# Optimization experiments

Hardware: AMD Instinct MI355X
Metric: run time of the kernel (lower is better)

Reference implementation:

```python
import jax, jax.numpy as jnp
import numpy as np

B, W, D, R = 8, 1024, 1024, 64
GAMMA_MIN, GAMMA_MAX, ALPHA_CAP, EPS = 0.15, 1.0, 1.0, 1e-8


def _linear_init(key, fan_in, shape):
    bound = 1.0 / np.sqrt(fan_in)
    return jax.random.uniform(key, shape, jnp.float32, -bound, bound)


def setup_inputs() -> dict:
    key = jax.random.key(0)
    ks = jax.random.split(key, 12)
    h = jax.random.normal(ks[0], (B, W, D), jnp.float32)
    # k_base init as in __init__: exp(-0.15*max(j-i,0)) * tril, row-normalized
    pos = jnp.arange(W, dtype=jnp.float32)
    dist_ji = jnp.clip(pos[None, :] - pos[:, None], 0.0)
    causal = jnp.tril(jnp.ones((W, W), jnp.float32))
    k_init = jnp.exp(-0.15 * dist_ji) * causal
    k_base = k_init / jnp.clip(k_init.sum(axis=1, keepdims=True), 1e-8)
    # decay_logit init: gammas in [0.95, 0.995] -> inverse sigmoid of normalized gamma
    gammas = jnp.linspace(0.95, 0.995, R)
    graw = jnp.clip((gammas - GAMMA_MIN) / (GAMMA_MAX - GAMMA_MIN), 1e-6, 1 - 1e-6)
    decay_logit = jnp.log(graw / (1.0 - graw))
    return {
        "h": h,
        "k_base": k_base,
        "decay_logit": decay_logit,
        "gate_logit": jnp.asarray(8.0, jnp.float32),
        "alpha_logit": jnp.asarray(0.0, jnp.float32),
        "u": 0.05 * jax.random.normal(ks[1], (D, R), jnp.float32),
        "v": 0.05 * jax.random.normal(ks[2], (D, R), jnp.float32),
        "proj_w": _linear_init(ks[3], D, (D, D)),
        "proj_b": _linear_init(ks[4], D, (D,)),
        "norm1_scale": jnp.ones((D,), jnp.float32),
        "norm2_scale": jnp.ones((D,), jnp.float32),
        "up_w": _linear_init(ks[5], D, (2 * D, D)),
        "up_b": _linear_init(ks[6], D, (2 * D,)),
        "down_w": _linear_init(ks[7], 2 * D, (D, 2 * D)),
        "down_b": _linear_init(ks[8], 2 * D, (D,)),
    }


def _rmsnorm(x, scale):
    return x * jax.lax.rsqrt(jnp.mean(x * x, axis=-1, keepdims=True) + 1e-8) * scale


def _l2norm(x):
    # mirrors F.normalize(x, dim=-1, eps=1e-8)
    n = jnp.sqrt(jnp.sum(x * x, axis=-1, keepdims=True))
    return x / jnp.maximum(n, EPS)


def reference(h, k_base, decay_logit, gate_logit, alpha_logit, u, v,
              proj_w, proj_b, norm1_scale, norm2_scale,
              up_w, up_b, down_w, down_b):
    _, w, _ = h.shape
    pos = jnp.arange(w, dtype=h.dtype)
    causal = jnp.tril(jnp.ones((w, w), h.dtype))          # [W, W]
    dist = jnp.clip(pos[:, None] - pos[None, :], 0.0)     # i - j, clamped >= 0

    residual = h
    h_norm = _rmsnorm(h, norm1_scale)

    # dense k_base path (k_base_rank == 0)
    gate = jax.nn.sigmoid(gate_logit)
    kb = k_base[:w, :w] * causal
    out = gate * jnp.einsum('ij,bjd->bid', kb, h_norm)

    # low-rank q/k with per-rank gamma decay (decay_impl='mask')
    qk = h_norm @ jnp.concatenate((u, v), axis=1)          # [B, W, 2R]
    q_raw, k_raw = jnp.split(qk, [u.shape[1]], axis=-1)
    q = _l2norm(q_raw)
    k = _l2norm(k_raw)

    gamma = GAMMA_MIN + (GAMMA_MAX - GAMMA_MIN) * jax.nn.sigmoid(decay_logit)  # [R]
    log_gamma = jnp.log(jnp.clip(gamma, 1e-8))
    decay_mask = jnp.exp(dist[:, :, None] * log_gamma[None, None, :]) * causal[:, :, None]  # [W, W, R]

    alpha = ALPHA_CAP * jax.nn.sigmoid(alpha_logit)
    # scores[b,i,j] = sum_r q[b,i,r] * decay[i,j,r] * k[b,j,r]
    scores = jnp.einsum('bir,ijr,bjr->bij', q, decay_mask, k)
    out = out + alpha * jnp.einsum('bij,bjd->bid', scores, h_norm)

    h1 = residual + (out @ proj_w.T + proj_b)
    # MLP (GELU exact, mult=2), second residual
    m = _rmsnorm(h1, norm2_scale)
    m = jax.nn.gelu(m @ up_w.T + up_b, approximate=False) @ down_w.T + down_b
    return h1 + m
```

## Files before the change

### kernel.cpp

```cpp
#include <hip/hip_runtime.h>
#include <hip/hip_bf16.h>
#include <math.h>

#define B_ 8
#define W_ 1024
#define D_ 1024
#define R_ 64

typedef __hip_bfloat16 bf16;
typedef __attribute__((ext_vector_type(8))) short bf16x8;
typedef __attribute__((ext_vector_type(4))) float f32x4;

__device__ __forceinline__ float tof(bf16 x) { return __bfloat162float(x); }
__device__ __forceinline__ short f2bs(float f) {
    bf16 b = __float2bfloat16(f);
    return *(short*)&b;
}

__device__ __forceinline__ void async16(const void* g, void* l) {
    __builtin_amdgcn_global_load_lds(
        (const __attribute__((address_space(1))) unsigned int*)g,
        (__attribute__((address_space(3))) unsigned int*)l,
        16, 0, 0);
}

__global__ __launch_bounds__(256)
void rmsnorm_kernel(const float* __restrict__ src, const float* __restrict__ scale,
                    bf16* __restrict__ dst) {
    int row = blockIdx.x;
    const float* x = src + (size_t)row * D_;
    bf16* y = dst + (size_t)row * D_;
    float xv[4];
    float ss = 0.f;
#pragma unroll
    for (int it = 0; it < 4; ++it) {
        int d = threadIdx.x + it * 256;
        xv[it] = x[d];
        ss += xv[it] * xv[it];
    }
#pragma unroll
    for (int off = 32; off; off >>= 1) ss += __shfl_down(ss, off, 64);
    __shared__ float red[4];
    __shared__ float invs;
    int lane = threadIdx.x & 63, wid = threadIdx.x >> 6;
    if (lane == 0) red[wid] = ss;
    __syncthreads();
    if (threadIdx.x == 0) {
        float t = red[0] + red[1] + red[2] + red[3];
        invs = rsqrtf(t / (float)D_ + 1e-8f);
    }
    __syncthreads();
    float inv = invs;
#pragma unroll
    for (int it = 0; it < 4; ++it) {
        int d = threadIdx.x + it * 256;
        y[d] = __float2bfloat16(xv[it] * inv * scale[d]);
    }
}

__global__ __launch_bounds__(256)
void transpose_kernel(const bf16* __restrict__ src, bf16* __restrict__ dst) {
    int b = blockIdx.z;
    int j0 = blockIdx.x * 64, d0 = blockIdx.y * 64;
    __shared__ short Ts[64][72];
    const bf16* S = src + (size_t)b * W_ * D_;
    bf16* Dd = dst + (size_t)b * W_ * D_;
    int tid = threadIdx.x;
    int r = tid >> 3, c = (tid & 7) * 8;
#pragma unroll
    for (int p = 0; p < 2; ++p) {
        int j = r + p * 32;
        bf16x8 vv = *(const bf16x8*)&S[(size_t)(j0 + j) * D_ + d0 + c];
#pragma unroll
        for (int e = 0; e < 8; ++e) Ts[j][c + e] = vv[e];
    }
    __syncthreads();
#pragma unroll
    for (int p = 0; p < 2; ++p) {
        int d = r + p * 32;
        bf16x8 vv;
#pragma unroll
        for (int e = 0; e < 8; ++e) vv[e] = Ts[c + e][d];
        *(bf16x8*)&Dd[(size_t)(d0 + d) * W_ + j0 + c] = vv;
    }
}

__global__ __launch_bounds__(256)
void uvT_kernel(const float* __restrict__ u, const float* __restrict__ v,
                bf16* __restrict__ uvT) {
    int g = blockIdx.z;
    int d0 = blockIdx.x * 64;
    const float* src = g ? v : u;
    __shared__ float Ts[64][65];
    int tid = threadIdx.x;
#pragma unroll
    for (int e = 0; e < 16; ++e) {
        int idx = tid + e * 256;
        int drow = idx >> 6, rcol = idx & 63;
        Ts[drow][rcol] = src[(size_t)(d0 + drow) * 64 + rcol];
    }
    __syncthreads();
#pragma unroll
    for (int e = 0; e < 16; ++e) {
        int idx = tid + e * 256;
        int orow = idx >> 6, ocol = idx & 63;
        uvT[(size_t)(g * 64 + orow) * D_ + d0 + ocol] = __float2bfloat16(Ts[ocol][orow]);
    }
}

__global__ __launch_bounds__(256)
void convert_kernel(const float* __restrict__ src, bf16* __restrict__ dst, int n) {
    int idx = (blockIdx.x * 256 + threadIdx.x) * 8;
    if (idx >= n) return;
    float4 f0 = *(const float4*)(src + idx);
    float4 f1 = *(const float4*)(src + idx + 4);
    bf16x8 p;
    p[0] = f2bs(f0.x); p[1] = f2bs(f0.y); p[2] = f2bs(f0.z); p[3] = f2bs(f0.w);
    p[4] = f2bs(f1.x); p[5] = f2bs(f1.y); p[6] = f2bs(f1.z); p[7] = f2bs(f1.w);
    *(bf16x8*)(dst + idx) = p;
}

__global__ __launch_bounds__(128)
void qk_epilogue_kernel(const bf16* __restrict__ qkraw,
                        const float* __restrict__ decay_logit,
                        float* __restrict__ qg, float* __restrict__ kg) {
    int row = blockIdx.x;
    int i = row & (W_ - 1);
    int t = threadIdx.x;
    int r = t & 63;
    bool isK = t >= 64;
    float val = tof(qkraw[(size_t)row * 128 + t]);
    float sq = val * val;
#pragma unroll
    for (int off = 32; off; off >>= 1) sq += __shfl_xor(sq, off, 64);
    val = val / fmaxf(sqrtf(sq), 1e-8f);

    float dl = decay_logit[r];
    float gamma = 0.15f + 0.85f * (1.f / (1.f + expf(-dl)));
    float lg = logf(gamma);
    float e = isK ? expf(-(float)i * lg) : expf((float)i * lg);
    float o = val * e;
    if (isK) kg[(size_t)row * R_ + r] = o;
    else     qg[(size_t)row * R_ + r] = o;
}

__global__ __launch_bounds__(256)
void buildM_kernel(const float* __restrict__ qg, const float* __restrict__ kg,
                   const float* __restrict__ k_base,
                   const float* __restrict__ gate_logit,
                   const float* __restrict__ alpha_logit,
                   bf16* __restrict__ M) {
    int b = blockIdx.z;
    int ti = blockIdx.y, tj = blockIdx.x;
    int i0 = ti * 32, j0 = tj * 32;
    int tx = threadIdx.x, ty = threadIdx.y;
    bf16* Mb = M + (size_t)b * W_ * W_;
    const bf16 zero = __float2bfloat16(0.f);

    if (tj > ti) {
#pragma unroll
        for (int a = 0; a < 2; ++a)
#pragma unroll
            for (int c = 0; c < 2; ++c)
                Mb[(size_t)(i0 + ty * 2 + a) * W_ + (j0 + tx * 2 + c)] = zero;
        return;
    }

    __shared__ float Qs[32][65];
    __shared__ float Ks[32][65];
    int tid = ty * 16 + tx;
    for (int e = tid; e < 32 * 64; e += 256) {
        int rr = e & 63, row = e >> 6;
        Qs[row][rr] = qg[((size_t)b * W_ + i0 + row) * R_ + rr];
        Ks[row][rr] = kg[((size_t)b * W_ + j0 + row) * R_ + rr];
    }
    __syncthreads();

    float acc[2][2] = {{0.f, 0.f}, {0.f, 0.f}};
#pragma unroll 8
    for (int r = 0; r < 64; ++r) {
        float qa = Qs[ty * 2 + 0][r], qb = Qs[ty * 2 + 1][r];
        float ka = Ks[tx * 2 + 0][r], kb = Ks[tx * 2 + 1][r];
        acc[0][0] += qa * ka; acc[0][1] += qa * kb;
        acc[1][0] += qb * ka; acc[1][1] += qb * kb;
    }

    float gate  = 1.f / (1.f + expf(-(*gate_logit)));
    float alpha = 1.f / (1.f + expf(-(*alpha_logit)));
#pragma unroll
    for (int a = 0; a < 2; ++a) {
#pragma unroll
        for (int c = 0; c < 2; ++c) {
            int i = i0 + ty * 2 + a, j = j0 + tx * 2 + c;
            float vkb = k_base[(size_t)i * W_ + j];
            float out = (j <= i) ? (gate * vkb + alpha * acc[a][c]) : 0.f;
            Mb[(size_t)i * W_ + j] = __float2bfloat16(out);
        }
    }
}

template<int EPI>
__global__ __launch_bounds__(256)
void mgemm_kernel(const bf16* __restrict__ A, const bf16* __restrict__ Bm,
                  const float* __restrict__ Res, const float* __restrict__ bias,
                  void* __restrict__ Cout,
                  int M, int N, int K,
                  long sA, long sB, long sC, int causal) {
    __shared__ __align__(16) short At[2][128 * 32];
    __shared__ __align__(16) short Bt[2][128 * 32];
    const bf16* Ab = A + (size_t)blockIdx.z * sA;
    const bf16* Bb = Bm + (size_t)blockIdx.z * sB;
    int m0 = blockIdx.y * 128, n0 = blockIdx.x * 128;
    int tid = threadIdx.x;
    int lane = tid & 63, wave = tid >> 6;
    int wy = wave >> 1, wx = wave & 1;
    int quad = lane >> 4, l15 = lane & 15;

    f32x4 acc[4][4];
#pragma unroll
    for (int i = 0; i < 4; ++i)
#pragma unroll
        for (int j = 0; j < 4; ++j)
            acc[i][j] = (f32x4){0.f, 0.f, 0.f, 0.f};

    int kmax = causal ? (m0 + 128 < K ? m0 + 128 : K) : K;
    int nIter = kmax >> 5;

    int srcChunk = ((lane & 3) ^ ((lane >> 3) & 3)) * 8;
    size_t rowA = (size_t)(m0 + wave * 16 + (lane >> 2)) * K;
    size_t rowB = (size_t)(n0 + wave * 16 + (lane >> 2)) * K;
    const bf16* aP0 = Ab + rowA + srcChunk;
    const bf16* aP1 = aP0 + (size_t)64 * K;
    const bf16* bP0 = Bb + rowB + srcChunk;
    const bf16* bP1 = bP0 + (size_t)64 * K;
    short* dA0[2] = { &At[0][wave * 512],        &At[1][wave * 512] };
    short* dA1[2] = { &At[0][2048 + wave * 512], &At[1][2048 + wave * 512] };
    short* dB0[2] = { &Bt[0][wave * 512],        &Bt[1][wave * 512] };
    short* dB1[2] = { &Bt[0][2048 + wave * 512], &Bt[1][2048 + wave * 512] };

    int rswz = (quad ^ ((l15 >> 1) & 3)) * 8;

    async16(aP0, dA0[0]); async16(aP1, dA1[0]);
    async16(bP0, dB0[0]); async16(bP1, dB1[0]);
    aP0 += 32; aP1 += 32; bP0 += 32; bP1 += 32;
    __syncthreads();

    for (int it = 0; it < nIter; ++it) {
        int cur = it & 1;
        if (it + 1 < nIter) {
            int nxt = cur ^ 1;
            async16(aP0, dA0[nxt]); async16(aP1, dA1[nxt]);
            async16(bP0, dB0[nxt]); async16(bP1, dB1[nxt]);
            aP0 += 32; aP1 += 32; bP0 += 32; bP1 += 32;
        }
        bf16x8 af[4], bfr[4];
#pragma unroll
        for (int mi = 0; mi < 4; ++mi)
            af[mi] = *(const bf16x8*)&At[cur][(wy * 64 + mi * 16 + l15) * 32 + rswz];
#pragma unroll
        for (int ni = 0; ni < 4; ++ni)
            bfr[ni] = *(const bf16x8*)&Bt[cur][(wx * 64 + ni * 16 + l15) * 32 + rswz];
#pragma unroll
        for (int mi = 0; mi < 4; ++mi)
#pragma unroll
            for (int ni = 0; ni < 4; ++ni)
                acc[mi][ni] = __builtin_amdgcn_mfma_f32_16x16x32_bf16(
                    af[mi], bfr[ni], acc[mi][ni], 0, 0, 0);
        __syncthreads();
    }

#pragma unroll
    for (int ni = 0; ni < 4; ++ni) {
        int col = n0 + wx * 64 + ni * 16 + l15;
        float bv = (EPI != 0) ? bias[col] : 0.f;
#pragma unroll
        for (int mi = 0; mi < 4; ++mi) {
            int row0 = m0 + wy * 64 + mi * 16 + quad * 4;
#pragma unroll
            for (int r = 0; r < 4; ++r) {
                size_t idx = (size_t)(row0 + r) * N + col;
                float val = acc[mi][ni][r];
                if constexpr (EPI == 0) {
                    ((bf16*)Cout)[(size_t)blockIdx.z * sC + idx] = __float2bfloat16(val);
                } else if constexpr (EPI == 1) {
                    ((float*)Cout)[idx] = val + bv + Res[idx];
                } else {
                    val += bv;
                    val = 0.5f * val * (1.f + erff(val * 0.70710678118654752f));
                    ((bf16*)Cout)[idx] = __float2bfloat16(val);
                }
            }
        }
    }
}

extern "C" void kernel_launch(void* const* d_in, const int* in_sizes, int n_in,
                              void* d_out, int out_size, void* d_ws, size_t ws_size,
                              hipStream_t stream) {
    const float* h           = (const float*)d_in[0];
    const float* k_base      = (const float*)d_in[1];
    const float* decay_logit = (const float*)d_in[2];
    const float* gate_logit  = (const float*)d_in[3];
    const float* alpha_logit = (const float*)d_in[4];
    const float* u           = (const float*)d_in[5];
    const float* v           = (const float*)d_in[6];
    const float* proj_w      = (const float*)d_in[7];
    const float* proj_b      = (const float*)d_in[8];
    const float* norm1_scale = (const float*)d_in[9];
    const float* norm2_scale = (const float*)d_in[10];
    const float* up_w        = (const float*)d_in[11];
    const float* up_b        = (const float*)d_in[12];
    const float* down_w      = (const float*)d_in[13];
    const float* down_b      = (const float*)d_in[14];

    const size_t MB = 1048576;
    char* ws = (char*)d_ws;
    bf16*  hnorm   = (bf16*)(ws);
    float* qg      = (float*)(ws + 16 * MB);
    float* kg      = (float*)(ws + 18 * MB);
    bf16*  hnormT  = (bf16*)(ws + 20 * MB);
    bf16*  Mbuf    = (bf16*)(ws + 36 * MB);
    bf16*  qkraw   = (bf16*)(ws + 36 * MB);
    bf16*  uvT     = (bf16*)(ws + 39 * MB);
    bf16*  proj_wb = (bf16*)(ws + 52 * MB);
    bf16*  up_wb   = (bf16*)(ws + 54 * MB);
    bf16*  down_wb = (bf16*)(ws + 58 * MB);
    bf16*  attn    = hnorm;
    bf16*  mnorm   = hnorm;
    bf16*  tbuf    = hnormT;
    float* h1      = (float*)d_out;

    convert_kernel<<<D_ * D_ / 2048, 256, 0, stream>>>(proj_w, proj_wb, D_ * D_);
    convert_kernel<<<2 * D_ * D_ / 2048, 256, 0, stream>>>(up_w, up_wb, 2 * D_ * D_);
    convert_kernel<<<2 * D_ * D_ / 2048, 256, 0, stream>>>(down_w, down_wb, 2 * D_ * D_);
    uvT_kernel<<<dim3(D_ / 64, 1, 2), 256, 0, stream>>>(u, v, uvT);

    rmsnorm_kernel<<<B_ * W_, 256, 0, stream>>>(h, norm1_scale, hnorm);

    transpose_kernel<<<dim3(W_ / 64, D_ / 64, B_), 256, 0, stream>>>(hnorm, hnormT);

    mgemm_kernel<0><<<dim3(1, B_ * W_ / 128, 1), 256, 0, stream>>>(
        hnorm, uvT, nullptr, nullptr, qkraw, B_ * W_, 128, D_, 0, 0, 0, 0);

    qk_epilogue_kernel<<<B_ * W_, 128, 0, stream>>>(qkraw, decay_logit, qg, kg);

    buildM_kernel<<<dim3(W_ / 32, W_ / 32, B_), dim3(16, 16), 0, stream>>>(
        qg, kg, k_base, gate_logit, alpha_logit, Mbuf);

    mgemm_kernel<0><<<dim3(D_ / 128, W_ / 128, B_), 256, 0, stream>>>(
        Mbuf, hnormT, nullptr, nullptr, attn, W_, D_, W_,
        (long)W_ * W_, (long)W_ * D_, (long)W_ * D_, 1);

    mgemm_kernel<1><<<dim3(D_ / 128, B_ * W_ / 128, 1), 256, 0, stream>>>(
        attn, proj_wb, h, proj_b, h1, B_ * W_, D_, D_, 0, 0, 0, 0);

    rmsnorm_kernel<<<B_ * W_, 256, 0, stream>>>(h1, norm2_scale, mnorm);

    mgemm_kernel<2><<<dim3(2 * D_ / 128, B_ * W_ / 128, 1), 256, 0, stream>>>(
        mnorm, up_wb, nullptr, up_b, tbuf, B_ * W_, 2 * D_, D_, 0, 0, 0, 0);

    mgemm_kernel<1><<<dim3(D_ / 128, B_ * W_ / 128, 1), 256, 0, stream>>>(
        tbuf, down_wb, h1, down_b, (float*)d_out, B_ * W_, D_, 2 * D_, 0, 0, 0, 0);
}
```

Before: 383.8 us.

## Use split-K with atomic accumulation for qk, proj and down GEMMs

Adds a split-K template parameter to the bf16 MFMA GEMM so the qk projection (4-way), the proj GEMM (2-way) and the down GEMM (2-way) spread K across blockIdx.z and accumulate fp32 results with atomicAdd. The output is seeded beforehand: a memset for qk, a new seed kernel that writes h+proj_b into h1, and for the down GEMM the existing h1 already in the output plus the bias added only by split 0. The aim is more blocks for the narrow qk GEMM (64 blocks before) and better occupancy overall. In exchange it adds atomic traffic, an extra seed pass over h, and makes the fp32 summation order nondeterministic.

```diff
diff --git a/kernel.cpp b/kernel.cpp
--- a/kernel.cpp
+++ b/kernel.cpp
@@ -120,8 +120,19 @@
     *(bf16x8*)(dst + idx) = p;
 }
 
+__global__ __launch_bounds__(256)
+void seed_kernel(const float* __restrict__ h, const float* __restrict__ bias,
+                 float* __restrict__ out) {
+    size_t idx = ((size_t)blockIdx.x * 256 + threadIdx.x) * 4;
+    int n = (int)(idx & (D_ - 1));
+    float4 hv = *(const float4*)(h + idx);
+    float4 bv = *(const float4*)(bias + n);
+    float4 o = { hv.x + bv.x, hv.y + bv.y, hv.z + bv.z, hv.w + bv.w };
+    *(float4*)(out + idx) = o;
+}
+
 __global__ __launch_bounds__(128)
-void qk_epilogue_kernel(const bf16* __restrict__ qkraw,
+void qk_epilogue_kernel(const float* __restrict__ qkraw,
                         const float* __restrict__ decay_logit,
                         float* __restrict__ qg, float* __restrict__ kg) {
     int row = blockIdx.x;
@@ -129,7 +140,7 @@
     int t = threadIdx.x;
     int r = t & 63;
     bool isK = t >= 64;
-    float val = tof(qkraw[(size_t)row * 128 + t]);
+    float val = qkraw[(size_t)row * 128 + t];
     float sq = val * val;
 #pragma unroll
     for (int off = 32; off; off >>= 1) sq += __shfl_xor(sq, off, 64);
@@ -199,17 +210,20 @@
     }
 }
 
-template<int EPI>
+template<int EPI, int SK>
 __global__ __launch_bounds__(256)
 void mgemm_kernel(const bf16* __restrict__ A, const bf16* __restrict__ Bm,
-                  const float* __restrict__ Res, const float* __restrict__ bias,
+                  const float* __restrict__ bias,
                   void* __restrict__ Cout,
                   int M, int N, int K,
                   long sA, long sB, long sC, int causal) {
     __shared__ __align__(16) short At[2][128 * 32];
     __shared__ __align__(16) short Bt[2][128 * 32];
-    const bf16* Ab = A + (size_t)blockIdx.z * sA;
-    const bf16* Bb = Bm + (size_t)blockIdx.z * sB;
+    int z = blockIdx.z;
+    const bf16* Ab = (SK > 1) ? A : A + (size_t)z * sA;
+    const bf16* Bb = (SK > 1) ? Bm : Bm + (size_t)z * sB;
+    int kchunk = K / SK;
+    int kbeg = (SK > 1) ? z * kchunk : 0;
     int m0 = blockIdx.y * 128, n0 = blockIdx.x * 128;
     int tid = threadIdx.x;
     int lane = tid & 63, wave = tid >> 6;
@@ -223,15 +237,16 @@
         for (int j = 0; j < 4; ++j)
             acc[i][j] = (f32x4){0.f, 0.f, 0.f, 0.f};
 
-    int kmax = causal ? (m0 + 128 < K ? m0 + 128 : K) : K;
-    int nIter = kmax >> 5;
+    int kend = kbeg + kchunk;
+    if (SK == 1 && causal) kend = (m0 + 128 < K) ? m0 + 128 : K;
+    int nIter = (kend - kbeg) >> 5;
 
     int srcChunk = ((lane & 3) ^ ((lane >> 3) & 3)) * 8;
     size_t rowA = (size_t)(m0 + wave * 16 + (lane >> 2)) * K;
     size_t rowB = (size_t)(n0 + wave * 16 + (lane >> 2)) * K;
-    const bf16* aP0 = Ab + rowA + srcChunk;
+    const bf16* aP0 = Ab + rowA + srcChunk + kbeg;
     const bf16* aP1 = aP0 + (size_t)64 * K;
-    const bf16* bP0 = Bb + rowB + srcChunk;
+    const bf16* bP0 = Bb + rowB + srcChunk + kbeg;
     const bf16* bP1 = bP0 + (size_t)64 * K;
     short* dA0[2] = { &At[0][wave * 512],        &At[1][wave * 512] };
     short* dA1[2] = { &At[0][2048 + wave * 512], &At[1][2048 + wave * 512] };
@@ -272,7 +287,8 @@
 #pragma unroll
     for (int ni = 0; ni < 4; ++ni) {
         int col = n0 + wx * 64 + ni * 16 + l15;
-        float bv = (EPI != 0) ? bias[col] : 0.f;
+        float bv = (EPI == 2 || EPI == 3) ? bias[col] : 0.f;
+        if (EPI == 3 && SK > 1 && z != 0) bv = 0.f;
 #pragma unroll
         for (int mi = 0; mi < 4; ++mi) {
             int row0 = m0 + wy * 64 + mi * 16 + quad * 4;
@@ -281,13 +297,15 @@
                 size_t idx = (size_t)(row0 + r) * N + col;
                 float val = acc[mi][ni][r];
                 if constexpr (EPI == 0) {
-                    ((bf16*)Cout)[(size_t)blockIdx.z * sC + idx] = __float2bfloat16(val);
-                } else if constexpr (EPI == 1) {
-                    ((float*)Cout)[idx] = val + bv + Res[idx];
-                } else {
+                    ((bf16*)Cout)[(size_t)z * sC + idx] = __float2bfloat16(val);
+                } else if constexpr (EPI == 2) {
                     val += bv;
                     val = 0.5f * val * (1.f + erff(val * 0.70710678118654752f));
                     ((bf16*)Cout)[idx] = __float2bfloat16(val);
+                } else if constexpr (EPI == 3) {
+                    atomicAdd(&((float*)Cout)[idx], val + bv);
+                } else {
+                    atomicAdd(&((float*)Cout)[idx], val);
                 }
             }
         }
@@ -319,9 +337,9 @@
     float* qg      = (float*)(ws + 16 * MB);
     float* kg      = (float*)(ws + 18 * MB);
     bf16*  hnormT  = (bf16*)(ws + 20 * MB);
+    float* qkraw   = (float*)(ws + 36 * MB);
+    bf16*  uvT     = (bf16*)(ws + 40 * MB);
     bf16*  Mbuf    = (bf16*)(ws + 36 * MB);
-    bf16*  qkraw   = (bf16*)(ws + 36 * MB);
-    bf16*  uvT     = (bf16*)(ws + 39 * MB);
     bf16*  proj_wb = (bf16*)(ws + 52 * MB);
     bf16*  up_wb   = (bf16*)(ws + 54 * MB);
     bf16*  down_wb = (bf16*)(ws + 58 * MB);
@@ -334,31 +352,33 @@
     convert_kernel<<<2 * D_ * D_ / 2048, 256, 0, stream>>>(up_w, up_wb, 2 * D_ * D_);
     convert_kernel<<<2 * D_ * D_ / 2048, 256, 0, stream>>>(down_w, down_wb, 2 * D_ * D_);
     uvT_kernel<<<dim3(D_ / 64, 1, 2), 256, 0, stream>>>(u, v, uvT);
+    hipMemsetAsync(qkraw, 0, (size_t)B_ * W_ * 128 * sizeof(float), stream);
 
     rmsnorm_kernel<<<B_ * W_, 256, 0, stream>>>(h, norm1_scale, hnorm);
 
     transpose_kernel<<<dim3(W_ / 64, D_ / 64, B_), 256, 0, stream>>>(hnorm, hnormT);
 
-    mgemm_kernel<0><<<dim3(1, B_ * W_ / 128, 1), 256, 0, stream>>>(
-        hnorm, uvT, nullptr, nullptr, qkraw, B_ * W_, 128, D_, 0, 0, 0, 0);
+    mgemm_kernel<4, 4><<<dim3(1, B_ * W_ / 128, 4), 256, 0, stream>>>(
+        hnorm, uvT, nullptr, qkraw, B_ * W_, 128, D_, 0, 0, 0, 0);
 
     qk_epilogue_kernel<<<B_ * W_, 128, 0, stream>>>(qkraw, decay_logit, qg, kg);
 
     buildM_kernel<<<dim3(W_ / 32, W_ / 32, B_), dim3(16, 16), 0, stream>>>(
         qg, kg, k_base, gate_logit, alpha_logit, Mbuf);
 
-    mgemm_kernel<0><<<dim3(D_ / 128, W_ / 128, B_), 256, 0, stream>>>(
-        Mbuf, hnormT, nullptr, nullptr, attn, W_, D_, W_,
+    mgemm_kernel<0, 1><<<dim3(D_ / 128, W_ / 128, B_), 256, 0, stream>>>(
+        Mbuf, hnormT, nullptr, attn, W_, D_, W_,
         (long)W_ * W_, (long)W_ * D_, (long)W_ * D_, 1);
 
-    mgemm_kernel<1><<<dim3(D_ / 128, B_ * W_ / 128, 1), 256, 0, stream>>>(
-        attn, proj_wb, h, proj_b, h1, B_ * W_, D_, D_, 0, 0, 0, 0);
+    seed_kernel<<<B_ * W_ * D_ / 1024, 256, 0, stream>>>(h, proj_b, h1);
+    mgemm_kernel<4, 2><<<dim3(D_ / 128, B_ * W_ / 128, 2), 256, 0, stream>>>(
+        attn, proj_wb, nullptr, h1, B_ * W_, D_, D_, 0, 0, 0, 0);
 
     rmsnorm_kernel<<<B_ * W_, 256, 0, stream>>>(h1, norm2_scale, mnorm);
 
-    mgemm_kernel<2><<<dim3(2 * D_ / 128, B_ * W_ / 128, 1), 256, 0, stream>>>(
-        mnorm, up_wb, nullptr, up_b, tbuf, B_ * W_, 2 * D_, D_, 0, 0, 0, 0);
-
-    mgemm_kernel<1><<<dim3(D_ / 128, B_ * W_ / 128, 1), 256, 0, stream>>>(
-        tbuf, down_wb, h1, down_b, (float*)d_out, B_ * W_, D_, 2 * D_, 0, 0, 0, 0);
-}
+    mgemm_kernel<2, 1><<<dim3(2 * D_ / 128, B_ * W_ / 128, 1), 256, 0, stream>>>(
+        mnorm, up_wb, up_b, tbuf, B_ * W_, 2 * D_, D_, 0, 0, 0, 0);
+
+    mgemm_kernel<3, 2><<<dim3(D_ / 128, B_ * W_ / 128, 2), 256, 0, stream>>>(
+        tbuf, down_wb, down_b, (float*)d_out, B_ * W_, D_, 2 * D_, 0, 0, 0, 0);
+}
```

Result: slower. 468.1 us (+22.0%).

## Add split-K for qk projection and narrow N tiles for small-grid GEMMs

Applied to the files above, without the earlier changes.

The qk projection GEMM (N=128) now uses split-K by 4 with 64-wide N tiles. It writes fp32 partial sums, and the qk epilogue kernel adds them together, so far more workgroups run on the device. The attention, projection and down GEMMs switch to 128x64 tiles to double their block counts and fill the CUs better. The cost is extra fp32 partial-sum traffic, less data reuse per tile, and a reshuffled workspace layout.

```diff
diff --git a/kernel.cpp b/kernel.cpp
--- a/kernel.cpp
+++ b/kernel.cpp
@@ -121,7 +121,7 @@
 }
 
 __global__ __launch_bounds__(128)
-void qk_epilogue_kernel(const bf16* __restrict__ qkraw,
+void qk_epilogue_kernel(const float* __restrict__ qkraw,
                         const float* __restrict__ decay_logit,
                         float* __restrict__ qg, float* __restrict__ kg) {
     int row = blockIdx.x;
@@ -129,10 +129,12 @@
     int t = threadIdx.x;
     int r = t & 63;
     bool isK = t >= 64;
-    float val = tof(qkraw[(size_t)row * 128 + t]);
+    const size_t PS = (size_t)B_ * W_ * 128;
+    size_t off = (size_t)row * 128 + t;
+    float val = qkraw[off] + qkraw[PS + off] + qkraw[2 * PS + off] + qkraw[3 * PS + off];
     float sq = val * val;
 #pragma unroll
-    for (int off = 32; off; off >>= 1) sq += __shfl_xor(sq, off, 64);
+    for (int o = 32; o; o >>= 1) sq += __shfl_xor(sq, o, 64);
     val = val / fmaxf(sqrtf(sq), 1e-8f);
 
     float dl = decay_logit[r];
@@ -199,49 +201,56 @@
     }
 }
 
-template<int EPI>
+template<int EPI, int SK, int BN>
 __global__ __launch_bounds__(256)
 void mgemm_kernel(const bf16* __restrict__ A, const bf16* __restrict__ Bm,
                   const float* __restrict__ Res, const float* __restrict__ bias,
                   void* __restrict__ Cout,
                   int M, int N, int K,
                   long sA, long sB, long sC, int causal) {
+    constexpr int WNT = BN / 32;
     __shared__ __align__(16) short At[2][128 * 32];
-    __shared__ __align__(16) short Bt[2][128 * 32];
-    const bf16* Ab = A + (size_t)blockIdx.z * sA;
-    const bf16* Bb = Bm + (size_t)blockIdx.z * sB;
-    int m0 = blockIdx.y * 128, n0 = blockIdx.x * 128;
+    __shared__ __align__(16) short Bt[2][BN * 32];
+    int z = blockIdx.z;
+    const bf16* Ab = (SK > 1) ? A : A + (size_t)z * sA;
+    const bf16* Bb = (SK > 1) ? Bm : Bm + (size_t)z * sB;
+    int kchunk = K / SK;
+    int kbeg = (SK > 1) ? z * kchunk : 0;
+    int m0 = blockIdx.y * 128, n0 = blockIdx.x * BN;
     int tid = threadIdx.x;
     int lane = tid & 63, wave = tid >> 6;
     int wy = wave >> 1, wx = wave & 1;
     int quad = lane >> 4, l15 = lane & 15;
 
-    f32x4 acc[4][4];
+    f32x4 acc[4][WNT];
 #pragma unroll
     for (int i = 0; i < 4; ++i)
 #pragma unroll
-        for (int j = 0; j < 4; ++j)
+        for (int j = 0; j < WNT; ++j)
             acc[i][j] = (f32x4){0.f, 0.f, 0.f, 0.f};
 
-    int kmax = causal ? (m0 + 128 < K ? m0 + 128 : K) : K;
-    int nIter = kmax >> 5;
+    int kend = kbeg + kchunk;
+    if (SK == 1 && causal) kend = (m0 + 128 < K) ? m0 + 128 : K;
+    int nIter = (kend - kbeg) >> 5;
 
     int srcChunk = ((lane & 3) ^ ((lane >> 3) & 3)) * 8;
     size_t rowA = (size_t)(m0 + wave * 16 + (lane >> 2)) * K;
     size_t rowB = (size_t)(n0 + wave * 16 + (lane >> 2)) * K;
-    const bf16* aP0 = Ab + rowA + srcChunk;
+    const bf16* aP0 = Ab + rowA + srcChunk + kbeg;
     const bf16* aP1 = aP0 + (size_t)64 * K;
-    const bf16* bP0 = Bb + rowB + srcChunk;
+    const bf16* bP0 = Bb + rowB + srcChunk + kbeg;
     const bf16* bP1 = bP0 + (size_t)64 * K;
     short* dA0[2] = { &At[0][wave * 512],        &At[1][wave * 512] };
     short* dA1[2] = { &At[0][2048 + wave * 512], &At[1][2048 + wave * 512] };
     short* dB0[2] = { &Bt[0][wave * 512],        &Bt[1][wave * 512] };
-    short* dB1[2] = { &Bt[0][2048 + wave * 512], &Bt[1][2048 + wave * 512] };
+    short* dB1[2] = { BN == 128 ? &Bt[0][2048 + wave * 512] : nullptr,
+                      BN == 128 ? &Bt[1][2048 + wave * 512] : nullptr };
 
     int rswz = (quad ^ ((l15 >> 1) & 3)) * 8;
 
     async16(aP0, dA0[0]); async16(aP1, dA1[0]);
-    async16(bP0, dB0[0]); async16(bP1, dB1[0]);
+    async16(bP0, dB0[0]);
+    if (BN == 128) async16(bP1, dB1[0]);
     aP0 += 32; aP1 += 32; bP0 += 32; bP1 += 32;
     __syncthreads();
 
@@ -250,29 +259,30 @@
         if (it + 1 < nIter) {
             int nxt = cur ^ 1;
             async16(aP0, dA0[nxt]); async16(aP1, dA1[nxt]);
-            async16(bP0, dB0[nxt]); async16(bP1, dB1[nxt]);
+            async16(bP0, dB0[nxt]);
+            if (BN == 128) async16(bP1, dB1[nxt]);
             aP0 += 32; aP1 += 32; bP0 += 32; bP1 += 32;
         }
-        bf16x8 af[4], bfr[4];
+        bf16x8 af[4], bfr[WNT];
 #pragma unroll
         for (int mi = 0; mi < 4; ++mi)
             af[mi] = *(const bf16x8*)&At[cur][(wy * 64 + mi * 16 + l15) * 32 + rswz];
 #pragma unroll
-        for (int ni = 0; ni < 4; ++ni)
-            bfr[ni] = *(const bf16x8*)&Bt[cur][(wx * 64 + ni * 16 + l15) * 32 + rswz];
+        for (int ni = 0; ni < WNT; ++ni)
+            bfr[ni] = *(const bf16x8*)&Bt[cur][(wx * (BN / 2) + ni * 16 + l15) * 32 + rswz];
 #pragma unroll
         for (int mi = 0; mi < 4; ++mi)
 #pragma unroll
-            for (int ni = 0; ni < 4; ++ni)
+            for (int ni = 0; ni < WNT; ++ni)
                 acc[mi][ni] = __builtin_amdgcn_mfma_f32_16x16x32_bf16(
                     af[mi], bfr[ni], acc[mi][ni], 0, 0, 0);
         __syncthreads();
     }
 
 #pragma unroll
-    for (int ni = 0; ni < 4; ++ni) {
-        int col = n0 + wx * 64 + ni * 16 + l15;
-        float bv = (EPI != 0) ? bias[col] : 0.f;
+    for (int ni = 0; ni < WNT; ++ni) {
+        int col = n0 + wx * (BN / 2) + ni * 16 + l15;
+        float bv = (EPI == 1 || EPI == 2) ? bias[col] : 0.f;
 #pragma unroll
         for (int mi = 0; mi < 4; ++mi) {
             int row0 = m0 + wy * 64 + mi * 16 + quad * 4;
@@ -281,13 +291,15 @@
                 size_t idx = (size_t)(row0 + r) * N + col;
                 float val = acc[mi][ni][r];
                 if constexpr (EPI == 0) {
-                    ((bf16*)Cout)[(size_t)blockIdx.z * sC + idx] = __float2bfloat16(val);
+                    ((bf16*)Cout)[(size_t)z * sC + idx] = __float2bfloat16(val);
                 } else if constexpr (EPI == 1) {
                     ((float*)Cout)[idx] = val + bv + Res[idx];
-                } else {
+                } else if constexpr (EPI == 2) {
                     val += bv;
                     val = 0.5f * val * (1.f + erff(val * 0.70710678118654752f));
                     ((bf16*)Cout)[idx] = __float2bfloat16(val);
+                } else {
+                    ((float*)Cout)[(size_t)z * sC + idx] = val;
                 }
             }
         }
@@ -316,12 +328,12 @@
     const size_t MB = 1048576;
     char* ws = (char*)d_ws;
     bf16*  hnorm   = (bf16*)(ws);
+    bf16*  uvT     = (bf16*)(ws + 16 * MB);
     float* qg      = (float*)(ws + 16 * MB);
     float* kg      = (float*)(ws + 18 * MB);
     bf16*  hnormT  = (bf16*)(ws + 20 * MB);
+    float* qkraw   = (float*)(ws + 36 * MB);
     bf16*  Mbuf    = (bf16*)(ws + 36 * MB);
-    bf16*  qkraw   = (bf16*)(ws + 36 * MB);
-    bf16*  uvT     = (bf16*)(ws + 39 * MB);
     bf16*  proj_wb = (bf16*)(ws + 52 * MB);
     bf16*  up_wb   = (bf16*)(ws + 54 * MB);
     bf16*  down_wb = (bf16*)(ws + 58 * MB);
@@ -339,26 +351,27 @@
 
     transpose_kernel<<<dim3(W_ / 64, D_ / 64, B_), 256, 0, stream>>>(hnorm, hnormT);
 
-    mgemm_kernel<0><<<dim3(1, B_ * W_ / 128, 1), 256, 0, stream>>>(
-        hnorm, uvT, nullptr, nullptr, qkraw, B_ * W_, 128, D_, 0, 0, 0, 0);
+    mgemm_kernel<5, 4, 64><<<dim3(2, B_ * W_ / 128, 4), 256, 0, stream>>>(
+        hnorm, uvT, nullptr, nullptr, qkraw, B_ * W_, 128, D_,
+        0, 0, (long)B_ * W_ * 128, 0);
 
     qk_epilogue_kernel<<<B_ * W_, 128, 0, stream>>>(qkraw, decay_logit, qg, kg);
 
     buildM_kernel<<<dim3(W_ / 32, W_ / 32, B_), dim3(16, 16), 0, stream>>>(
         qg, kg, k_base, gate_logit, alpha_logit, Mbuf);
 
-    mgemm_kernel<0><<<dim3(D_ / 128, W_ / 128, B_), 256, 0, stream>>>(
+    mgemm_kernel<0, 1, 64><<<dim3(D_ / 64, W_ / 128, B_), 256, 0, stream>>>(
         Mbuf, hnormT, nullptr, nullptr, attn, W_, D_, W_,
         (long)W_ * W_, (long)W_ * D_, (long)W_ * D_, 1);
 
-    mgemm_kernel<1><<<dim3(D_ / 128, B_ * W_ / 128, 1), 256, 0, stream>>>(
+    mgemm_kernel<1, 1, 64><<<dim3(D_ / 64, B_ * W_ / 128, 1), 256, 0, stream>>>(
         attn, proj_wb, h, proj_b, h1, B_ * W_, D_, D_, 0, 0, 0, 0);
 
     rmsnorm_kernel<<<B_ * W_, 256, 0, stream>>>(h1, norm2_scale, mnorm);
 
-    mgemm_kernel<2><<<dim3(2 * D_ / 128, B_ * W_ / 128, 1), 256, 0, stream>>>(
+    mgemm_kernel<2, 1, 128><<<dim3(2 * D_ / 128, B_ * W_ / 128, 1), 256, 0, stream>>>(
         mnorm, up_wb, nullptr, up_b, tbuf, B_ * W_, 2 * D_, D_, 0, 0, 0, 0);
 
-    mgemm_kernel<1><<<dim3(D_ / 128, B_ * W_ / 128, 1), 256, 0, stream>>>(
+    mgemm_kernel<1, 1, 64><<<dim3(D_ / 64, B_ * W_ / 128, 1), 256, 0, stream>>>(
         tbuf, down_wb, h1, down_b, (float*)d_out, B_ * W_, D_, 2 * D_, 0, 0, 0, 0);
 }
```

Result: slower. 411.1 us (+7.1%).
